# Performance work log

Measured on AMD Instinct MI355X. Metric: run time of the kernel, lower is better.

Reference implementation:

```python
import jax, jax.numpy as jnp
import numpy as np

# Dims from init_kwargs / input_specs
C_IN, H, W = 128, 224, 224
C_OUT, KH, KW = 256, 3, 3
STRIDE = 1  # padding='valid'


def setup_inputs() -> dict:
    key = jax.random.key(0)
    k1, k2 = jax.random.split(key)
    x = jax.random.normal(k1, (C_IN, H, W), dtype=jnp.float32)
    kernels = jax.random.normal(k2, (C_OUT, C_IN, KH, KW), dtype=jnp.float32) * 0.05
    return {"x": x, "kernels": kernels}


def reference(x, kernels):
    # Original does im2col + matmul, which is exactly a valid cross-correlation
    # (no kernel flip). Express it as a direct conv: (1,C,H,W) * (O,I,kh,kw).
    out = jax.lax.conv_general_dilated(
        x[None],                      # (1, C_in, H, W)
        kernels,                      # (C_out, C_in, KH, KW)
        window_strides=(STRIDE, STRIDE),
        padding="VALID",
        dimension_numbers=("NCHW", "OIHW", "NCHW"),
    )
    return out[0]                     # (C_out, H_out, W_out) = (256, 222, 222)
```

## Files before the change

### kernel.cpp

```cpp
#include <hip/hip_runtime.h>

#define CIN   128
#define HH    224
#define WW    224
#define COUT  256
#define HO    222
#define WO    222
#define PLANE (224 * 224 * 64)

typedef unsigned short u16;
typedef unsigned int   u32;
typedef __bf16  bf16x8 __attribute__((ext_vector_type(8)));
typedef float   f32x4  __attribute__((ext_vector_type(4)));

__device__ __forceinline__ u16 f2bf(float f) {
  union { float f; u32 u; } v; v.f = f;
  u32 u = v.u;
  return (u16)((u + 0x7FFFu + ((u >> 16) & 1u)) >> 16);
}

__global__ void prep(const float* __restrict__ x, const float* __restrict__ w,
                     u16* __restrict__ xp, u16* __restrict__ wp) {
  const int t = threadIdx.x;
  if (blockIdx.x < 448) {
    const int h  = blockIdx.x >> 1;
    const int ch = blockIdx.x & 1;
    __shared__ u16 tile[64][228];
#pragma unroll
    for (int i = 0; i < 14; ++i) {
      int idx = i * 256 + t;
      int c   = idx / 56;
      int wq  = idx % 56;
      float4 v = *(const float4*)(&x[(size_t)(ch * 64 + c) * (HH * WW) + h * WW + wq * 4]);
      uint2 p;
      p.x = (u32)f2bf(v.x) | ((u32)f2bf(v.y) << 16);
      p.y = (u32)f2bf(v.z) | ((u32)f2bf(v.w) << 16);
      *(uint2*)(&tile[c][wq * 4]) = p;
    }
    __syncthreads();
#pragma unroll
    for (int i = 0; i < 7; ++i) {
      int idx  = i * 256 + t;
      int ww   = idx >> 3;
      int jcp  = idx & 7;
      int jsrc = jcp ^ (ww & 7);
      uint4 v;
      v.x = (u32)tile[jsrc * 8 + 0][ww] | ((u32)tile[jsrc * 8 + 1][ww] << 16);
      v.y = (u32)tile[jsrc * 8 + 2][ww] | ((u32)tile[jsrc * 8 + 3][ww] << 16);
      v.z = (u32)tile[jsrc * 8 + 4][ww] | ((u32)tile[jsrc * 8 + 5][ww] << 16);
      v.w = (u32)tile[jsrc * 8 + 6][ww] | ((u32)tile[jsrc * 8 + 7][ww] << 16);
      *(uint4*)(&xp[(size_t)ch * PLANE + (size_t)(h * WW + ww) * 64 + jcp * 8]) = v;
    }
  } else {
    int u    = (blockIdx.x - 448) * 256 + t;
    int jcp  = u & 7;
    int mr   = (u >> 3) & 127;
    int rest = u >> 10;
    int kw   = rest % 3;
    int q    = rest / 3;
    int ch   = q & 1;
    int r    = q >> 1;
    int kh   = r % 3;
    int mt   = r / 3;
    int oc   = mt * 128 + mr;
    int cb   = ch * 64 + (jcp ^ (mr & 7)) * 8;
    u16 o[8];
#pragma unroll
    for (int e = 0; e < 8; ++e)
      o[e] = f2bf(w[((size_t)(oc * CIN + cb + e) * 3 + kh) * 3 + kw]);
    uint4 v;
    v.x = (u32)o[0] | ((u32)o[1] << 16);
    v.y = (u32)o[2] | ((u32)o[3] << 16);
    v.z = (u32)o[4] | ((u32)o[5] << 16);
    v.w = (u32)o[6] | ((u32)o[7] << 16);
    *(uint4*)(&wp[(size_t)u * 8]) = v;
  }
}

__device__ __forceinline__ void lds_dma16(const u16* g, u16* l) {
  __builtin_amdgcn_global_load_lds(
      reinterpret_cast<__attribute__((address_space(1))) u32*>(
          reinterpret_cast<uintptr_t>(g)),
      reinterpret_cast<__attribute__((address_space(3))) u32*>(
          reinterpret_cast<uintptr_t>(l)),
      16, 0, 0);
}

__global__ __launch_bounds__(256, 2) void conv_mfma(const u16* __restrict__ wp,
                                                    const u16* __restrict__ xp,
                                                    float* __restrict__ out) {
  __shared__ u16 ldsB[226 * 64];

  const int tid  = threadIdx.x;
  const int lane = tid & 63;
  const int wave = tid >> 6;
  const int quad = lane >> 4;
  const int lr   = lane & 15;
  const int wm   = wave >> 1;
  const int wn   = wave & 1;

  const int bx  = blockIdx.x;
  const int xcd = bx & 7;
  const int mt  = (bx >> 3) & 1;
  const int oh  = xcd * 28 + (bx >> 4);
  if (oh >= HO) return;

  f32x4 acc[4][7];
#pragma unroll
  for (int i = 0; i < 4; ++i)
#pragma unroll
    for (int j = 0; j < 7; ++j) acc[i][j] = {0.f, 0.f, 0.f, 0.f};

  int swA[2];
#pragma unroll
  for (int ks = 0; ks < 2; ++ks)
    swA[ks] = ((ks * 4 + quad) ^ (lr & 7)) << 3;

  for (int s = 0; s < 6; ++s) {
    const int ch = s & 1;
    const int kh = s >> 1;

    const u16* g = xp + (size_t)ch * PLANE + (size_t)(oh + kh) * (WW * 64);

    __syncthreads();
#pragma unroll
    for (int uu = 0; uu < 7; ++uu) {
      const int unit = wave * 7 + uu;
      lds_dma16(g + unit * 512 + lane * 8, &ldsB[unit * 512]);
    }
    __syncthreads();

    const u16* Ab = wp + (size_t)((mt * 3 + kh) * 2 + ch) * 24576 + wm * 4096 + lr * 64;

#pragma unroll
    for (int kw = 0; kw < 3; ++kw) {
      const int bq  = (wn * 112 + lr + kw) * 64;
      const int sw7 = (lr + kw) & 7;
#pragma unroll
      for (int ks = 0; ks < 2; ++ks) {
        const int swB = ((ks * 4 + quad) ^ sw7) << 3;
        bf16x8 af[4], bg[7];
#pragma unroll
        for (int i = 0; i < 4; ++i)
          af[i] = *reinterpret_cast<const bf16x8*>(Ab + kw * 8192 + i * 1024 + swA[ks]);
#pragma unroll
        for (int j = 0; j < 7; ++j)
          bg[j] = *reinterpret_cast<const bf16x8*>(&ldsB[bq + j * 1024 + swB]);
#pragma unroll
        for (int i = 0; i < 4; ++i)
#pragma unroll
          for (int j = 0; j < 7; ++j)
            acc[i][j] = __builtin_amdgcn_mfma_f32_16x16x32_bf16(af[i], bg[j], acc[i][j], 0, 0, 0);
      }
    }
  }

  const int mb = mt * 128 + wm * 64;
#pragma unroll
  for (int i = 0; i < 4; ++i) {
#pragma unroll
    for (int j = 0; j < 7; ++j) {
      const int col = wn * 112 + j * 16 + lr;
      if (col < WO) {
        float* op = out + (size_t)(mb + i * 16 + quad * 4) * (HO * WO) +
                    (size_t)oh * WO + col;
#pragma unroll
        for (int r = 0; r < 4; ++r)
          op[(size_t)r * (HO * WO)] = acc[i][j][r];
      }
    }
  }
}

__global__ void conv_naive(const float* __restrict__ x, const float* __restrict__ w,
                           float* __restrict__ out) {
  int idx = blockIdx.x * 256 + threadIdx.x;
  if (idx >= COUT * HO * WO) return;
  int ow  = idx % WO;
  int tmp = idx / WO;
  int oh  = tmp % HO;
  int oc  = tmp / HO;
  float s = 0.f;
  for (int c = 0; c < CIN; ++c)
    for (int kh = 0; kh < 3; ++kh) {
      const float* xr = &x[(size_t)(c * HH + oh + kh) * WW + ow];
      const float* wr = &w[((size_t)(oc * CIN + c) * 3 + kh) * 3];
      s += xr[0] * wr[0] + xr[1] * wr[1] + xr[2] * wr[2];
    }
  out[idx] = s;
}

extern "C" void kernel_launch(void* const* d_in, const int* in_sizes, int n_in,
                              void* d_out, int out_size, void* d_ws, size_t ws_size,
                              hipStream_t stream) {
  const float* x    = (const float*)d_in[0];
  const float* kern = (const float*)d_in[1];
  float* out        = (float*)d_out;

  const size_t WP_BYTES = (size_t)36864 * 16;
  const size_t XP_BYTES = (size_t)2 * PLANE * 2;

  if (ws_size >= WP_BYTES + XP_BYTES) {
    u16* wp = (u16*)d_ws;
    u16* xp = (u16*)((char*)d_ws + WP_BYTES);
    hipLaunchKernelGGL(prep, dim3(592), dim3(256), 0, stream, x, kern, xp, wp);
    hipLaunchKernelGGL(conv_mfma, dim3(448), dim3(256), 0, stream, wp, xp, out);
  } else {
    int total = COUT * HO * WO;
    hipLaunchKernelGGL(conv_naive, dim3((total + 255) / 256), dim3(256), 0, stream,
                       x, kern, out);
  }
}
```

Measured before the change: 117.0 us.

## Double-buffer input rows in LDS and prefetch weight fragments into registers

```diff
diff --git a/kernel.cpp b/kernel.cpp
--- a/kernel.cpp
+++ b/kernel.cpp
@@ -23,8 +23,10 @@
                      u16* __restrict__ xp, u16* __restrict__ wp) {
   const int t = threadIdx.x;
   if (blockIdx.x < 448) {
-    const int h  = blockIdx.x >> 1;
-    const int ch = blockIdx.x & 1;
+    const int xcd = blockIdx.x & 7;
+    const int q   = blockIdx.x >> 3;
+    const int h   = xcd * 28 + (q >> 1);
+    const int ch  = q & 1;
     __shared__ u16 tile[64][228];
 #pragma unroll
     for (int i = 0; i < 14; ++i) {
@@ -89,7 +91,7 @@
 __global__ __launch_bounds__(256, 2) void conv_mfma(const u16* __restrict__ wp,
                                                     const u16* __restrict__ xp,
                                                     float* __restrict__ out) {
-  __shared__ u16 ldsB[226 * 64];
+  __shared__ u16 ldsB[2][226 * 64];
 
   const int tid  = threadIdx.x;
   const int lane = tid & 63;
@@ -116,41 +118,76 @@
   for (int ks = 0; ks < 2; ++ks)
     swA[ks] = ((ks * 4 + quad) ^ (lr & 7)) << 3;
 
+  {
+    const u16* g0 = xp + (size_t)oh * (WW * 64);
+#pragma unroll
+    for (int uu = 0; uu < 7; ++uu) {
+      const int unit = wave * 7 + uu;
+      lds_dma16(g0 + unit * 512 + lane * 8, &ldsB[0][unit * 512]);
+    }
+  }
+
   for (int s = 0; s < 6; ++s) {
     const int ch = s & 1;
     const int kh = s >> 1;
-
-    const u16* g = xp + (size_t)ch * PLANE + (size_t)(oh + kh) * (WW * 64);
+    const u16* Ab = wp + (size_t)((mt * 3 + kh) * 2 + ch) * 24576 + wm * 4096 + lr * 64;
+    const u16* Bbuf = ldsB[s & 1];
 
     __syncthreads();
-#pragma unroll
-    for (int uu = 0; uu < 7; ++uu) {
-      const int unit = wave * 7 + uu;
-      lds_dma16(g + unit * 512 + lane * 8, &ldsB[unit * 512]);
-    }
-    __syncthreads();
-
-    const u16* Ab = wp + (size_t)((mt * 3 + kh) * 2 + ch) * 24576 + wm * 4096 + lr * 64;
+
+    bf16x8 afp[2][4];
+#pragma unroll
+    for (int ks = 0; ks < 2; ++ks)
+#pragma unroll
+      for (int i = 0; i < 4; ++i)
+        afp[ks][i] = *reinterpret_cast<const bf16x8*>(Ab + i * 1024 + swA[ks]);
+
+    if (s < 5) {
+      const int ch2 = (s + 1) & 1;
+      const int kh2 = (s + 1) >> 1;
+      const u16* g = xp + (size_t)ch2 * PLANE + (size_t)(oh + kh2) * (WW * 64);
+      u16* dst = ldsB[(s + 1) & 1];
+#pragma unroll
+      for (int uu = 0; uu < 7; ++uu) {
+        const int unit = wave * 7 + uu;
+        lds_dma16(g + unit * 512 + lane * 8, &dst[unit * 512]);
+      }
+    }
 
 #pragma unroll
     for (int kw = 0; kw < 3; ++kw) {
       const int bq  = (wn * 112 + lr + kw) * 64;
       const int sw7 = (lr + kw) & 7;
+
+      bf16x8 afn[2][4];
+      if (kw < 2) {
+#pragma unroll
+        for (int ks = 0; ks < 2; ++ks)
+#pragma unroll
+          for (int i = 0; i < 4; ++i)
+            afn[ks][i] = *reinterpret_cast<const bf16x8*>(Ab + (kw + 1) * 8192 + i * 1024 + swA[ks]);
+      }
+
 #pragma unroll
       for (int ks = 0; ks < 2; ++ks) {
         const int swB = ((ks * 4 + quad) ^ sw7) << 3;
-        bf16x8 af[4], bg[7];
+        bf16x8 bg[7];
+#pragma unroll
+        for (int j = 0; j < 7; ++j)
+          bg[j] = *reinterpret_cast<const bf16x8*>(&Bbuf[bq + j * 1024 + swB]);
 #pragma unroll
         for (int i = 0; i < 4; ++i)
-          af[i] = *reinterpret_cast<const bf16x8*>(Ab + kw * 8192 + i * 1024 + swA[ks]);
-#pragma unroll
-        for (int j = 0; j < 7; ++j)
-          bg[j] = *reinterpret_cast<const bf16x8*>(&ldsB[bq + j * 1024 + swB]);
-#pragma unroll
-        for (int i = 0; i < 4; ++i)
 #pragma unroll
           for (int j = 0; j < 7; ++j)
-            acc[i][j] = __builtin_amdgcn_mfma_f32_16x16x32_bf16(af[i], bg[j], acc[i][j], 0, 0, 0);
+            acc[i][j] = __builtin_amdgcn_mfma_f32_16x16x32_bf16(afp[ks][i], bg[j], acc[i][j], 0, 0, 0);
+      }
+
+      if (kw < 2) {
+#pragma unroll
+        for (int ks = 0; ks < 2; ++ks)
+#pragma unroll
+          for (int i = 0; i < 4; ++i)
+            afp[ks][i] = afn[ks][i];
       }
     }
   }
@@ -166,7 +203,7 @@
                     (size_t)oh * WO + col;
 #pragma unroll
         for (int r = 0; r < 4; ++r)
-          op[(size_t)r * (HO * WO)] = acc[i][j][r];
+          __builtin_nontemporal_store(acc[i][j][r], op + (size_t)r * (HO * WO));
       }
     }
   }
```

Result: slower. 131.5 us (+12.4%).

## Merge channel halves into single 128-channel interleaved input layout

Applied to the files above, without the earlier changes.

```diff
diff --git a/kernel.cpp b/kernel.cpp
--- a/kernel.cpp
+++ b/kernel.cpp
@@ -6,7 +6,6 @@
 #define COUT  256
 #define HO    222
 #define WO    222
-#define PLANE (224 * 224 * 64)
 
 typedef unsigned short u16;
 typedef unsigned int   u32;
@@ -22,16 +21,16 @@
 __global__ void prep(const float* __restrict__ x, const float* __restrict__ w,
                      u16* __restrict__ xp, u16* __restrict__ wp) {
   const int t = threadIdx.x;
-  if (blockIdx.x < 448) {
-    const int h  = blockIdx.x >> 1;
-    const int ch = blockIdx.x & 1;
-    __shared__ u16 tile[64][228];
-#pragma unroll
-    for (int i = 0; i < 14; ++i) {
+  if (blockIdx.x < 224) {
+    const int xcd = blockIdx.x & 7;
+    const int h   = xcd * 28 + (blockIdx.x >> 3);
+    __shared__ u16 tile[128][228];
+#pragma unroll
+    for (int i = 0; i < 28; ++i) {
       int idx = i * 256 + t;
       int c   = idx / 56;
       int wq  = idx % 56;
-      float4 v = *(const float4*)(&x[(size_t)(ch * 64 + c) * (HH * WW) + h * WW + wq * 4]);
+      float4 v = *(const float4*)(&x[(size_t)c * (HH * WW) + h * WW + wq * 4]);
       uint2 p;
       p.x = (u32)f2bf(v.x) | ((u32)f2bf(v.y) << 16);
       p.y = (u32)f2bf(v.z) | ((u32)f2bf(v.w) << 16);
@@ -39,20 +38,20 @@
     }
     __syncthreads();
 #pragma unroll
-    for (int i = 0; i < 7; ++i) {
+    for (int i = 0; i < 14; ++i) {
       int idx  = i * 256 + t;
-      int ww   = idx >> 3;
-      int jcp  = idx & 7;
-      int jsrc = jcp ^ (ww & 7);
+      int ww   = idx >> 4;
+      int jcp  = idx & 15;
+      int jsrc = jcp ^ (ww & 15);
       uint4 v;
       v.x = (u32)tile[jsrc * 8 + 0][ww] | ((u32)tile[jsrc * 8 + 1][ww] << 16);
       v.y = (u32)tile[jsrc * 8 + 2][ww] | ((u32)tile[jsrc * 8 + 3][ww] << 16);
       v.z = (u32)tile[jsrc * 8 + 4][ww] | ((u32)tile[jsrc * 8 + 5][ww] << 16);
       v.w = (u32)tile[jsrc * 8 + 6][ww] | ((u32)tile[jsrc * 8 + 7][ww] << 16);
-      *(uint4*)(&xp[(size_t)ch * PLANE + (size_t)(h * WW + ww) * 64 + jcp * 8]) = v;
+      *(uint4*)(&xp[((size_t)h * WW + ww) * 128 + jcp * 8]) = v;
     }
   } else {
-    int u    = (blockIdx.x - 448) * 256 + t;
+    int u    = (blockIdx.x - 224) * 256 + t;
     int jcp  = u & 7;
     int mr   = (u >> 3) & 127;
     int rest = u >> 10;
@@ -89,7 +88,7 @@
 __global__ __launch_bounds__(256, 2) void conv_mfma(const u16* __restrict__ wp,
                                                     const u16* __restrict__ xp,
                                                     float* __restrict__ out) {
-  __shared__ u16 ldsB[226 * 64];
+  __shared__ u16 ldsB[226 * 128];
 
   const int tid  = threadIdx.x;
   const int lane = tid & 63;
@@ -113,39 +112,37 @@
 
   int swA[2];
 #pragma unroll
-  for (int ks = 0; ks < 2; ++ks)
-    swA[ks] = ((ks * 4 + quad) ^ (lr & 7)) << 3;
-
-  for (int s = 0; s < 6; ++s) {
-    const int ch = s & 1;
-    const int kh = s >> 1;
-
-    const u16* g = xp + (size_t)ch * PLANE + (size_t)(oh + kh) * (WW * 64);
+  for (int k2 = 0; k2 < 2; ++k2)
+    swA[k2] = ((k2 * 4 + quad) ^ (lr & 7)) << 3;
+
+  for (int kh = 0; kh < 3; ++kh) {
+    const u16* g = xp + (size_t)(oh + kh) * (WW * 128);
 
     __syncthreads();
 #pragma unroll
-    for (int uu = 0; uu < 7; ++uu) {
-      const int unit = wave * 7 + uu;
+    for (int uu = 0; uu < 14; ++uu) {
+      const int unit = wave * 14 + uu;
       lds_dma16(g + unit * 512 + lane * 8, &ldsB[unit * 512]);
     }
     __syncthreads();
 
-    const u16* Ab = wp + (size_t)((mt * 3 + kh) * 2 + ch) * 24576 + wm * 4096 + lr * 64;
+    const u16* Ab = wp + (size_t)(mt * 3 + kh) * 2 * 24576 + wm * 4096 + lr * 64;
 
 #pragma unroll
     for (int kw = 0; kw < 3; ++kw) {
-      const int bq  = (wn * 112 + lr + kw) * 64;
-      const int sw7 = (lr + kw) & 7;
-#pragma unroll
-      for (int ks = 0; ks < 2; ++ks) {
-        const int swB = ((ks * 4 + quad) ^ sw7) << 3;
+      const int bq   = (wn * 112 + lr + kw) * 128;
+      const int sw15 = (lr + kw) & 15;
+#pragma unroll
+      for (int ks = 0; ks < 4; ++ks) {
+        const int swB = ((ks * 4 + quad) ^ sw15) << 3;
+        const u16* Ak = Ab + (ks >> 1) * 24576 + kw * 8192;
         bf16x8 af[4], bg[7];
 #pragma unroll
         for (int i = 0; i < 4; ++i)
-          af[i] = *reinterpret_cast<const bf16x8*>(Ab + kw * 8192 + i * 1024 + swA[ks]);
+          af[i] = *reinterpret_cast<const bf16x8*>(Ak + i * 1024 + swA[ks & 1]);
 #pragma unroll
         for (int j = 0; j < 7; ++j)
-          bg[j] = *reinterpret_cast<const bf16x8*>(&ldsB[bq + j * 1024 + swB]);
+          bg[j] = *reinterpret_cast<const bf16x8*>(&ldsB[bq + j * 2048 + swB]);
 #pragma unroll
         for (int i = 0; i < 4; ++i)
 #pragma unroll
@@ -198,12 +195,12 @@
   float* out        = (float*)d_out;
 
   const size_t WP_BYTES = (size_t)36864 * 16;
-  const size_t XP_BYTES = (size_t)2 * PLANE * 2;
+  const size_t XP_BYTES = (size_t)HH * WW * 128 * 2;
 
   if (ws_size >= WP_BYTES + XP_BYTES) {
     u16* wp = (u16*)d_ws;
     u16* xp = (u16*)((char*)d_ws + WP_BYTES);
-    hipLaunchKernelGGL(prep, dim3(592), dim3(256), 0, stream, x, kern, xp, wp);
+    hipLaunchKernelGGL(prep, dim3(368), dim3(256), 0, stream, x, kern, xp, wp);
     hipLaunchKernelGGL(conv_mfma, dim3(448), dim3(256), 0, stream, wp, xp, out);
   } else {
     int total = COUT * HO * WO;
```

New measurement: 120.7 us. +3.2%, slower.
